# Kernel tuning notes

Hardware: AMD Instinct MI355X
Metric: run time of the kernel (lower is better)

## Reference

```python
import jax, jax.numpy as jnp
import numpy as np
from jax import lax

B, VLEN, H, DIM, C = 32, 2048, 1024, 1024, 32  # batch, value len, hidden_dim, dim, conv_out_channel


def setup_inputs() -> dict:
    key = jax.random.key(0)
    ks = jax.random.split(key, 13)
    s = 0.02
    return {
        "query": jax.random.normal(ks[0], (B, 1, H), dtype=jnp.float32),
        "value": jax.random.normal(ks[1], (B, VLEN, H), dtype=jnp.float32),
        "prev_attn": jax.random.uniform(ks[2], (B, VLEN), dtype=jnp.float32),
        "conv_w": jax.random.normal(ks[3], (C, 1, 3), dtype=jnp.float32) * s,   # Conv1d weight (out,in,k)
        "conv_b": jax.random.normal(ks[4], (C,), dtype=jnp.float32) * s,
        "w_loc": jax.random.normal(ks[5], (DIM, C), dtype=jnp.float32) * s,     # loc_projection (no bias)
        "w_q": jax.random.normal(ks[6], (DIM, H), dtype=jnp.float32) * s,       # query_projection (no bias)
        "w_v": jax.random.normal(ks[7], (DIM, H), dtype=jnp.float32) * s,       # value_projection (no bias)
        "bias": jax.random.uniform(ks[8], (DIM,), dtype=jnp.float32, minval=-0.1, maxval=0.1),
        "w_score": jax.random.normal(ks[9], (1, DIM), dtype=jnp.float32) * s,   # score_projection weight
        "b_score": jax.random.normal(ks[10], (1,), dtype=jnp.float32) * s,
        "w_out": jax.random.normal(ks[11], (H, 2 * H), dtype=jnp.float32) * s,  # out_projection weight
        "b_out": jax.random.normal(ks[12], (H,), dtype=jnp.float32) * s,
    }


def reference(query, value, prev_attn, conv_w, conv_b, w_loc, w_q, w_v, bias,
              w_score, b_score, w_out, b_out):
    # Location features: Conv1d(1 -> C, k=3, pad=1) over prev_attn, then transpose to (B, V, C)
    conv = lax.conv_general_dilated(
        prev_attn[:, None, :], conv_w, window_strides=(1,), padding=[(1, 1)],
        dimension_numbers=("NCH", "OIH", "NCH"),
    ) + conv_b[None, :, None]                       # (B, C, V)
    conv_feat = jnp.transpose(conv, (0, 2, 1))      # (B, V, C)

    qp = jnp.einsum("bqh,dh->bqd", query, w_q)      # (B, 1, DIM)
    vp = jnp.einsum("bvh,dh->bvd", value, w_v)      # (B, V, DIM)
    lp = jnp.einsum("bvc,dc->bvd", conv_feat, w_loc)

    e = jnp.tanh(qp + vp + lp + bias)               # (B, V, DIM), qp broadcasts over V
    score = jnp.einsum("bvd,d->bv", e, w_score[0]) + b_score[0]  # (B, V)

    # smoothing=True: sigmoid then normalize
    s = jax.nn.sigmoid(score)
    attn = s / jnp.sum(s, axis=-1, keepdims=True)   # (B, V)

    context = jnp.einsum("bv,bvh->bh", attn, value)               # (B, H)
    combined = jnp.concatenate([context[:, None, :], query], axis=2)  # (B, 1, 2H)
    output = jnp.einsum("bqk,hk->bqh", combined, w_out) + b_out       # (B, 1, H)
    return output, attn
```

## Files before the change

kernel.cpp:

```cpp
#include <hip/hip_runtime.h>
#include <hip/hip_bf16.h>
#include <math.h>

#define B_SZ 32
#define VLEN_SZ 2048
#define H_SZ 1024
#define DIM_SZ 1024
#define C_SZ 32

typedef float f32x4 __attribute__((ext_vector_type(4)));
typedef short s16x8 __attribute__((ext_vector_type(8)));
typedef short s16x4 __attribute__((ext_vector_type(4)));

__device__ __forceinline__ short f2bf(float f) {
  unsigned u = __float_as_uint(f);
  u = (u + 0x7fffu + ((u >> 16) & 1u)) >> 16;
  return (short)u;
}

__device__ __forceinline__ float bf2f(short s) {
  return __uint_as_float(((unsigned)(unsigned short)s) << 16);
}

__device__ __forceinline__ float fast_tanh(float x) {
  float z = __expf(2.0f * x);
  return 1.0f - 2.0f / (z + 1.0f);
}

__device__ __forceinline__ void ldg_lds16(const short* g, short* l) {
  __builtin_amdgcn_global_load_lds(
      (const __attribute__((address_space(1))) unsigned int*)g,
      (__attribute__((address_space(3))) unsigned int*)l, 16, 0, 0);
}

__global__ __launch_bounds__(256) void k_prep(
    const float* __restrict__ query, const float* __restrict__ w_q,
    const float* __restrict__ bias, const float* __restrict__ prev,
    const float* __restrict__ conv_w, const float* __restrict__ conv_b,
    const float* __restrict__ w_loc, const float* __restrict__ w_v,
    const float* __restrict__ value,
    float* __restrict__ qpb, short* __restrict__ cfb, short* __restrict__ wlocb,
    short* __restrict__ wvb, short* __restrict__ vb,
    float* __restrict__ score, float* __restrict__ context) {
  int bid = blockIdx.x;
  int t = threadIdx.x;
  if (bid < 8192) {
    int wid = bid * 4 + (t >> 6);
    int lane = t & 63;
    int d = wid >> 5;
    int b = wid & 31;
    const f32x4* q4 = (const f32x4*)(query + (size_t)b * H_SZ);
    const f32x4* w4 = (const f32x4*)(w_q + (size_t)d * H_SZ);
    float acc = 0.f;
#pragma unroll
    for (int it = 0; it < 4; ++it) {
      int k = it * 64 + lane;
      f32x4 a = q4[k], w = w4[k];
      acc += a[0] * w[0] + a[1] * w[1] + a[2] * w[2] + a[3] * w[3];
    }
#pragma unroll
    for (int off = 32; off; off >>= 1) acc += __shfl_xor(acc, off, 64);
    if (lane == 0) qpb[(size_t)b * DIM_SZ + d] = acc + bias[d];
  } else if (bid < 8448) {
    int r = (bid - 8192) * 256 + t;
    int v = r & (VLEN_SZ - 1);
    float p0 = prev[r];
    float pm = (v > 0) ? prev[r - 1] : 0.f;
    float pp = (v < VLEN_SZ - 1) ? prev[r + 1] : 0.f;
#pragma unroll
    for (int c = 0; c < C_SZ; ++c) {
      float f = conv_b[c] + pm * conv_w[c * 3 + 0] + p0 * conv_w[c * 3 + 1] + pp * conv_w[c * 3 + 2];
      cfb[(size_t)r * C_SZ + c] = f2bf(f);
    }
  } else if (bid < 8480) {
    int i = (bid - 8448) * 256 + t;
    f32x4 v = ((const f32x4*)w_loc)[i];
    s16x4 o;
    o[0] = f2bf(v[0]); o[1] = f2bf(v[1]); o[2] = f2bf(v[2]); o[3] = f2bf(v[3]);
    ((s16x4*)wlocb)[i] = o;
  } else if (bid < 9504) {
    int i = (bid - 8480) * 256 + t;
    f32x4 v = ((const f32x4*)w_v)[i];
    s16x4 o;
    o[0] = f2bf(v[0]); o[1] = f2bf(v[1]); o[2] = f2bf(v[2]); o[3] = f2bf(v[3]);
    ((s16x4*)wvb)[i] = o;
  } else if (bid < 9568) {
    int i = (bid - 9504) * 256 + t;
    ((f32x4*)score)[i] = (f32x4){0.f, 0.f, 0.f, 0.f};
  } else if (bid < 9600) {
    int i = (bid - 9568) * 256 + t;
    ((f32x4*)context)[i] = (f32x4){0.f, 0.f, 0.f, 0.f};
  } else {
    size_t i = (size_t)(bid - 9600) * 256 + t;
    f32x4 x0 = ((const f32x4*)value)[2 * i];
    f32x4 x1 = ((const f32x4*)value)[2 * i + 1];
    s16x8 o;
    o[0] = f2bf(x0[0]); o[1] = f2bf(x0[1]); o[2] = f2bf(x0[2]); o[3] = f2bf(x0[3]);
    o[4] = f2bf(x1[0]); o[5] = f2bf(x1[1]); o[6] = f2bf(x1[2]); o[7] = f2bf(x1[3]);
    ((s16x8*)vb)[i] = o;
  }
}

__global__ __launch_bounds__(256, 3) void k_score(
    const short* __restrict__ vb, const short* __restrict__ wvb,
    const short* __restrict__ wlocb, const short* __restrict__ cfb,
    const float* __restrict__ qpb, const float* __restrict__ w_score,
    float* __restrict__ score) {
  __shared__ short As[128 * 32];
  __shared__ short Bs[128 * 32];
  __shared__ float sred[4][64];

  int t = threadIdx.x;
  int w = t >> 6, l = t & 63;
  int q = l >> 4, l16 = l & 15;
  int bid = blockIdx.x;
  int x = bid & 7;
  int j = bid >> 3;
  int nt = j & 7;
  int mt = x * 64 + (j >> 3);
  int row0 = mt * 128;
  int d0 = nt * 128;
  int b = row0 >> 11;
  int wm = w >> 1, wn = w & 1;

  int lr = l >> 2;
  int kc = ((l & 3) ^ ((l >> 3) & 3)) * 8;

  const short* gA0 = vb + (size_t)(row0 + 32 * w + lr) * H_SZ + kc;
  const short* gA1 = vb + (size_t)(row0 + 32 * w + 16 + lr) * H_SZ + kc;
  const short* gB0 = wvb + (size_t)(d0 + 32 * w + lr) * H_SZ + kc;
  const short* gB1 = wvb + (size_t)(d0 + 32 * w + 16 + lr) * H_SZ + kc;
  short* lA0 = As + (32 * w) * 32;
  short* lA1 = As + (32 * w + 16) * 32;
  short* lB0 = Bs + (32 * w) * 32;
  short* lB1 = Bs + (32 * w + 16) * 32;

  int posA = (q ^ ((l16 >> 1) & 3)) * 8;

  f32x4 acc[4][4];
#pragma unroll
  for (int i = 0; i < 4; ++i)
#pragma unroll
    for (int jj = 0; jj < 4; ++jj) acc[i][jj] = (f32x4){0.f, 0.f, 0.f, 0.f};

  for (int kt = 0; kt <= 32; ++kt) {
    if (kt < 32) {
      int k0 = kt * 32;
      ldg_lds16(gA0 + k0, lA0);
      ldg_lds16(gA1 + k0, lA1);
      ldg_lds16(gB0 + k0, lB0);
      ldg_lds16(gB1 + k0, lB1);
    } else {
      ldg_lds16(cfb + (size_t)(row0 + 32 * w + lr) * C_SZ + kc, lA0);
      ldg_lds16(cfb + (size_t)(row0 + 32 * w + 16 + lr) * C_SZ + kc, lA1);
      ldg_lds16(wlocb + (size_t)(d0 + 32 * w + lr) * C_SZ + kc, lB0);
      ldg_lds16(wlocb + (size_t)(d0 + 32 * w + 16 + lr) * C_SZ + kc, lB1);
    }
    __syncthreads();

    s16x8 a[4], bb[4];
#pragma unroll
    for (int i = 0; i < 4; ++i)
      a[i] = *(const s16x8*)(As + (wm * 64 + i * 16 + l16) * 32 + posA);
#pragma unroll
    for (int jj = 0; jj < 4; ++jj)
      bb[jj] = *(const s16x8*)(Bs + (wn * 64 + jj * 16 + l16) * 32 + posA);
#pragma unroll
    for (int i = 0; i < 4; ++i)
#pragma unroll
      for (int jj = 0; jj < 4; ++jj)
        acc[i][jj] = __builtin_amdgcn_mfma_f32_16x16x32_bf16(a[i], bb[jj], acc[i][jj], 0, 0, 0);
    __syncthreads();
  }

  float qv[4], wv[4];
#pragma unroll
  for (int jj = 0; jj < 4; ++jj) {
    int d = d0 + wn * 64 + jj * 16 + l16;
    qv[jj] = qpb[(size_t)b * DIM_SZ + d];
    wv[jj] = w_score[d];
  }

#pragma unroll
  for (int i = 0; i < 4; ++i) {
#pragma unroll
    for (int r = 0; r < 4; ++r) {
      float part = 0.f;
#pragma unroll
      for (int jj = 0; jj < 4; ++jj)
        part += fast_tanh(acc[i][jj][r] + qv[jj]) * wv[jj];
      part += __shfl_xor(part, 1);
      part += __shfl_xor(part, 2);
      part += __shfl_xor(part, 4);
      part += __shfl_xor(part, 8);
      if (l16 == 0) sred[w][i * 16 + q * 4 + r] = part;
    }
  }
  __syncthreads();
  if (t < 128) {
    int half = t >> 6;
    float v = sred[half * 2][t & 63] + sred[half * 2 + 1][t & 63];
    atomicAdd(&score[row0 + t], v);
  }
}

__global__ __launch_bounds__(256) void k_ctx(
    const float* __restrict__ score, const float* __restrict__ b_score,
    const short* __restrict__ vb, float* __restrict__ attn_out,
    float* __restrict__ context) {
  __shared__ float als[VLEN_SZ];
  __shared__ float red[4];
  int b = blockIdx.x, vc = blockIdx.y, t = threadIdx.x;
  float bs = b_score[0];
  float sv[8];
  float lsum = 0.f;
  int v0 = t * 8;
#pragma unroll
  for (int k = 0; k < 8; ++k) {
    float ps = score[(size_t)b * VLEN_SZ + v0 + k] + bs;
    float s = 1.0f / (1.0f + __expf(-ps));
    sv[k] = s;
    lsum += s;
    als[v0 + k] = s;
  }
#pragma unroll
  for (int off = 32; off; off >>= 1) lsum += __shfl_xor(lsum, off, 64);
  if ((t & 63) == 0) red[t >> 6] = lsum;
  __syncthreads();
  float inv = 1.0f / (red[0] + red[1] + red[2] + red[3]);
  if (vc == 0) {
#pragma unroll
    for (int k = 0; k < 8; ++k)
      attn_out[(size_t)b * VLEN_SZ + v0 + k] = sv[k] * inv;
  }

  int p = t >> 7, tt = t & 127, h0 = tt * 8;
  int vbase = vc * 512 + p * 256;
  const short* vp = vb + ((size_t)b * VLEN_SZ + vbase) * H_SZ + h0;
  const float* av = als + vbase;
  float acc[8] = {0.f, 0.f, 0.f, 0.f, 0.f, 0.f, 0.f, 0.f};
#pragma unroll 4
  for (int v = 0; v < 256; ++v) {
    s16x8 xv = *(const s16x8*)(vp + (size_t)v * H_SZ);
    float a = av[v];
#pragma unroll
    for (int k = 0; k < 8; ++k) acc[k] += a * bf2f(xv[k]);
  }
#pragma unroll
  for (int k = 0; k < 8; ++k)
    atomicAdd(&context[(size_t)b * H_SZ + h0 + k], acc[k] * inv);
}

__global__ void k_out(const float* __restrict__ context, const float* __restrict__ query,
                      const float* __restrict__ w_out, const float* __restrict__ b_out,
                      float* __restrict__ out) {
  int wid = blockIdx.x * 4 + (threadIdx.x >> 6);
  int lane = threadIdx.x & 63;
  int h = wid >> 5;
  int b = wid & 31;
  const f32x4* w4 = (const f32x4*)(w_out + (size_t)h * 2048);
  const f32x4* c4 = (const f32x4*)(context + (size_t)b * H_SZ);
  const f32x4* q4 = (const f32x4*)(query + (size_t)b * H_SZ);
  float acc = 0.f;
#pragma unroll
  for (int it = 0; it < 8; ++it) {
    int k4 = it * 64 + lane;
    f32x4 w = w4[k4];
    f32x4 c = (k4 < 256) ? c4[k4] : q4[k4 - 256];
    acc += w[0] * c[0] + w[1] * c[1] + w[2] * c[2] + w[3] * c[3];
  }
#pragma unroll
  for (int off = 32; off; off >>= 1) acc += __shfl_xor(acc, off, 64);
  if (lane == 0) out[(size_t)b * H_SZ + h] = acc + b_out[h];
}

extern "C" void kernel_launch(void* const* d_in, const int* in_sizes, int n_in,
                              void* d_out, int out_size, void* d_ws, size_t ws_size,
                              hipStream_t stream) {
  const float* query   = (const float*)d_in[0];
  const float* value   = (const float*)d_in[1];
  const float* prev    = (const float*)d_in[2];
  const float* conv_w  = (const float*)d_in[3];
  const float* conv_b  = (const float*)d_in[4];
  const float* w_loc   = (const float*)d_in[5];
  const float* w_q     = (const float*)d_in[6];
  const float* w_v     = (const float*)d_in[7];
  const float* bias    = (const float*)d_in[8];
  const float* w_score = (const float*)d_in[9];
  const float* b_score = (const float*)d_in[10];
  const float* w_out   = (const float*)d_in[11];
  const float* b_out   = (const float*)d_in[12];

  float* out  = (float*)d_out;
  float* attn = out + B_SZ * H_SZ;

  char* ws = (char*)d_ws;
  float* score   = (float*)(ws);
  float* qpb     = (float*)(ws + (256 << 10));
  float* context = (float*)(ws + (384 << 10));
  short* wvb     = (short*)(ws + (512 << 10));
  short* wlocb   = (short*)(ws + (2560 << 10));
  short* cfb     = (short*)(ws + (3 << 20));
  short* vb      = (short*)(ws + (8 << 20));

  k_prep<<<42368, 256, 0, stream>>>(query, w_q, bias, prev, conv_w, conv_b,
                                    w_loc, w_v, value,
                                    qpb, cfb, wlocb, wvb, vb, score, context);
  k_score<<<4096, 256, 0, stream>>>(vb, wvb, wlocb, cfb, qpb, w_score, score);
  k_ctx<<<dim3(B_SZ, 4), 256, 0, stream>>>(score, b_score, vb, attn, context);
  k_out<<<(B_SZ * H_SZ) / 4, 256, 0, stream>>>(context, query, w_out, b_out, out);
}
```

Before: 637.7 us.

## Drop bf16 value pre-conversion; load fp32 value directly into score GEMM

Removes the separate pass that converted the whole value tensor to bf16 in the prep kernel. The score GEMM now streams fp32 value tiles into LDS and packs them to bf16 by truncation when forming the MFMA operands. The context kernel reads fp32 value directly with a doubled grid. The aim is to avoid writing and re-reading a large bf16 copy, at the cost of double the LDS footprint and A-tile global traffic in the GEMM, plus truncation instead of round-to-nearest.

```diff
diff --git a/kernel.cpp b/kernel.cpp
--- a/kernel.cpp
+++ b/kernel.cpp
@@ -11,6 +11,7 @@
 typedef float f32x4 __attribute__((ext_vector_type(4)));
 typedef short s16x8 __attribute__((ext_vector_type(8)));
 typedef short s16x4 __attribute__((ext_vector_type(4)));
+typedef unsigned int u32x4 __attribute__((ext_vector_type(4)));
 
 __device__ __forceinline__ short f2bf(float f) {
   unsigned u = __float_as_uint(f);
@@ -22,12 +23,16 @@
   return __uint_as_float(((unsigned)(unsigned short)s) << 16);
 }
 
+__device__ __forceinline__ unsigned pack2(float a, float b) {
+  return __builtin_amdgcn_perm(__float_as_uint(b), __float_as_uint(a), 0x07060302u);
+}
+
 __device__ __forceinline__ float fast_tanh(float x) {
   float z = __expf(2.0f * x);
   return 1.0f - 2.0f / (z + 1.0f);
 }
 
-__device__ __forceinline__ void ldg_lds16(const short* g, short* l) {
+__device__ __forceinline__ void ldg_lds16(const void* g, void* l) {
   __builtin_amdgcn_global_load_lds(
       (const __attribute__((address_space(1))) unsigned int*)g,
       (__attribute__((address_space(3))) unsigned int*)l, 16, 0, 0);
@@ -38,10 +43,8 @@
     const float* __restrict__ bias, const float* __restrict__ prev,
     const float* __restrict__ conv_w, const float* __restrict__ conv_b,
     const float* __restrict__ w_loc, const float* __restrict__ w_v,
-    const float* __restrict__ value,
-    float* __restrict__ qpb, short* __restrict__ cfb, short* __restrict__ wlocb,
-    short* __restrict__ wvb, short* __restrict__ vb,
-    float* __restrict__ score, float* __restrict__ context) {
+    float* __restrict__ qpb, float* __restrict__ cff, short* __restrict__ wlocb,
+    short* __restrict__ wvb, float* __restrict__ score, float* __restrict__ context) {
   int bid = blockIdx.x;
   int t = threadIdx.x;
   if (bid < 8192) {
@@ -67,11 +70,14 @@
     float p0 = prev[r];
     float pm = (v > 0) ? prev[r - 1] : 0.f;
     float pp = (v < VLEN_SZ - 1) ? prev[r + 1] : 0.f;
-#pragma unroll
-    for (int c = 0; c < C_SZ; ++c) {
-      float f = conv_b[c] + pm * conv_w[c * 3 + 0] + p0 * conv_w[c * 3 + 1] + pp * conv_w[c * 3 + 2];
-      cfb[(size_t)r * C_SZ + c] = f2bf(f);
-    }
+    float o[C_SZ];
+#pragma unroll
+    for (int c = 0; c < C_SZ; ++c)
+      o[c] = conv_b[c] + pm * conv_w[c * 3 + 0] + p0 * conv_w[c * 3 + 1] + pp * conv_w[c * 3 + 2];
+    f32x4* dst = (f32x4*)(cff + (size_t)r * C_SZ);
+#pragma unroll
+    for (int g = 0; g < 8; ++g)
+      dst[g] = (f32x4){o[4 * g], o[4 * g + 1], o[4 * g + 2], o[4 * g + 3]};
   } else if (bid < 8480) {
     int i = (bid - 8448) * 256 + t;
     f32x4 v = ((const f32x4*)w_loc)[i];
@@ -87,26 +93,18 @@
   } else if (bid < 9568) {
     int i = (bid - 9504) * 256 + t;
     ((f32x4*)score)[i] = (f32x4){0.f, 0.f, 0.f, 0.f};
-  } else if (bid < 9600) {
+  } else {
     int i = (bid - 9568) * 256 + t;
     ((f32x4*)context)[i] = (f32x4){0.f, 0.f, 0.f, 0.f};
-  } else {
-    size_t i = (size_t)(bid - 9600) * 256 + t;
-    f32x4 x0 = ((const f32x4*)value)[2 * i];
-    f32x4 x1 = ((const f32x4*)value)[2 * i + 1];
-    s16x8 o;
-    o[0] = f2bf(x0[0]); o[1] = f2bf(x0[1]); o[2] = f2bf(x0[2]); o[3] = f2bf(x0[3]);
-    o[4] = f2bf(x1[0]); o[5] = f2bf(x1[1]); o[6] = f2bf(x1[2]); o[7] = f2bf(x1[3]);
-    ((s16x8*)vb)[i] = o;
-  }
-}
-
-__global__ __launch_bounds__(256, 3) void k_score(
-    const short* __restrict__ vb, const short* __restrict__ wvb,
-    const short* __restrict__ wlocb, const short* __restrict__ cfb,
+  }
+}
+
+__global__ __launch_bounds__(256, 4) void k_score(
+    const float* __restrict__ value, const short* __restrict__ wvb,
+    const short* __restrict__ wlocb, const float* __restrict__ cff,
     const float* __restrict__ qpb, const float* __restrict__ w_score,
     float* __restrict__ score) {
-  __shared__ short As[128 * 32];
+  __shared__ float As[128 * 32];
   __shared__ short Bs[128 * 32];
   __shared__ float sred[4][64];
 
@@ -123,19 +121,26 @@
   int b = row0 >> 11;
   int wm = w >> 1, wn = w & 1;
 
+  int ar = l >> 3;
+  int ac = (l & 7) ^ ar;
+  const float* gA[4];
+  float* lA[4];
+#pragma unroll
+  for (int s = 0; s < 4; ++s) {
+    gA[s] = value + (size_t)(row0 + 32 * w + 8 * s + ar) * H_SZ + ac * 4;
+    lA[s] = As + (32 * w + 8 * s) * 32;
+  }
   int lr = l >> 2;
   int kc = ((l & 3) ^ ((l >> 3) & 3)) * 8;
-
-  const short* gA0 = vb + (size_t)(row0 + 32 * w + lr) * H_SZ + kc;
-  const short* gA1 = vb + (size_t)(row0 + 32 * w + 16 + lr) * H_SZ + kc;
   const short* gB0 = wvb + (size_t)(d0 + 32 * w + lr) * H_SZ + kc;
   const short* gB1 = wvb + (size_t)(d0 + 32 * w + 16 + lr) * H_SZ + kc;
-  short* lA0 = As + (32 * w) * 32;
-  short* lA1 = As + (32 * w + 16) * 32;
   short* lB0 = Bs + (32 * w) * 32;
   short* lB1 = Bs + (32 * w + 16) * 32;
 
-  int posA = (q ^ ((l16 >> 1) & 3)) * 8;
+  int h7 = l16 & 7;
+  int pA0 = ((2 * q) ^ h7) * 4;
+  int pA1 = ((2 * q + 1) ^ h7) * 4;
+  int posB = (q ^ ((l16 >> 1) & 3)) * 8;
 
   f32x4 acc[4][4];
 #pragma unroll
@@ -146,13 +151,14 @@
   for (int kt = 0; kt <= 32; ++kt) {
     if (kt < 32) {
       int k0 = kt * 32;
-      ldg_lds16(gA0 + k0, lA0);
-      ldg_lds16(gA1 + k0, lA1);
-      ldg_lds16(gB0 + k0, lB0);
-      ldg_lds16(gB1 + k0, lB1);
+#pragma unroll
+      for (int s = 0; s < 4; ++s) ldg_lds16(gA[s] + k0, lA[s]);
+      ldg_lds16(gB0 + (size_t)k0, lB0);
+      ldg_lds16(gB1 + (size_t)k0, lB1);
     } else {
-      ldg_lds16(cfb + (size_t)(row0 + 32 * w + lr) * C_SZ + kc, lA0);
-      ldg_lds16(cfb + (size_t)(row0 + 32 * w + 16 + lr) * C_SZ + kc, lA1);
+#pragma unroll
+      for (int s = 0; s < 4; ++s)
+        ldg_lds16(cff + (size_t)(row0 + 32 * w + 8 * s + ar) * C_SZ + ac * 4, lA[s]);
       ldg_lds16(wlocb + (size_t)(d0 + 32 * w + lr) * C_SZ + kc, lB0);
       ldg_lds16(wlocb + (size_t)(d0 + 32 * w + 16 + lr) * C_SZ + kc, lB1);
     }
@@ -160,11 +166,20 @@
 
     s16x8 a[4], bb[4];
 #pragma unroll
-    for (int i = 0; i < 4; ++i)
-      a[i] = *(const s16x8*)(As + (wm * 64 + i * 16 + l16) * 32 + posA);
+    for (int i = 0; i < 4; ++i) {
+      const float* rowp = As + (wm * 64 + i * 16 + l16) * 32;
+      f32x4 f0 = *(const f32x4*)(rowp + pA0);
+      f32x4 f1 = *(const f32x4*)(rowp + pA1);
+      u32x4 pk;
+      pk[0] = pack2(f0[0], f0[1]);
+      pk[1] = pack2(f0[2], f0[3]);
+      pk[2] = pack2(f1[0], f1[1]);
+      pk[3] = pack2(f1[2], f1[3]);
+      a[i] = *(s16x8*)&pk;
+    }
 #pragma unroll
     for (int jj = 0; jj < 4; ++jj)
-      bb[jj] = *(const s16x8*)(Bs + (wn * 64 + jj * 16 + l16) * 32 + posA);
+      bb[jj] = *(const s16x8*)(Bs + (wn * 64 + jj * 16 + l16) * 32 + posB);
 #pragma unroll
     for (int i = 0; i < 4; ++i)
 #pragma unroll
@@ -206,7 +221,7 @@
 
 __global__ __launch_bounds__(256) void k_ctx(
     const float* __restrict__ score, const float* __restrict__ b_score,
-    const short* __restrict__ vb, float* __restrict__ attn_out,
+    const float* __restrict__ value, float* __restrict__ attn_out,
     float* __restrict__ context) {
   __shared__ float als[VLEN_SZ];
   __shared__ float red[4];
@@ -234,20 +249,20 @@
       attn_out[(size_t)b * VLEN_SZ + v0 + k] = sv[k] * inv;
   }
 
-  int p = t >> 7, tt = t & 127, h0 = tt * 8;
-  int vbase = vc * 512 + p * 256;
-  const short* vp = vb + ((size_t)b * VLEN_SZ + vbase) * H_SZ + h0;
+  int h0 = t * 4;
+  int vbase = vc * 256;
+  const float* vp = value + ((size_t)b * VLEN_SZ + vbase) * H_SZ + h0;
   const float* av = als + vbase;
-  float acc[8] = {0.f, 0.f, 0.f, 0.f, 0.f, 0.f, 0.f, 0.f};
-#pragma unroll 4
+  f32x4 acc = (f32x4){0.f, 0.f, 0.f, 0.f};
+#pragma unroll 8
   for (int v = 0; v < 256; ++v) {
-    s16x8 xv = *(const s16x8*)(vp + (size_t)v * H_SZ);
+    f32x4 xv = *(const f32x4*)(vp + (size_t)v * H_SZ);
     float a = av[v];
-#pragma unroll
-    for (int k = 0; k < 8; ++k) acc[k] += a * bf2f(xv[k]);
-  }
-#pragma unroll
-  for (int k = 0; k < 8; ++k)
+    acc[0] += a * xv[0]; acc[1] += a * xv[1];
+    acc[2] += a * xv[2]; acc[3] += a * xv[3];
+  }
+#pragma unroll
+  for (int k = 0; k < 4; ++k)
     atomicAdd(&context[(size_t)b * H_SZ + h0 + k], acc[k] * inv);
 }
 
@@ -300,13 +315,11 @@
   float* context = (float*)(ws + (384 << 10));
   short* wvb     = (short*)(ws + (512 << 10));
   short* wlocb   = (short*)(ws + (2560 << 10));
-  short* cfb     = (short*)(ws + (3 << 20));
-  short* vb      = (short*)(ws + (8 << 20));
-
-  k_prep<<<42368, 256, 0, stream>>>(query, w_q, bias, prev, conv_w, conv_b,
-                                    w_loc, w_v, value,
-                                    qpb, cfb, wlocb, wvb, vb, score, context);
-  k_score<<<4096, 256, 0, stream>>>(vb, wvb, wlocb, cfb, qpb, w_score, score);
-  k_ctx<<<dim3(B_SZ, 4), 256, 0, stream>>>(score, b_score, vb, attn, context);
+  float* cff     = (float*)(ws + (3 << 20));
+
+  k_prep<<<9600, 256, 0, stream>>>(query, w_q, bias, prev, conv_w, conv_b,
+                                   w_loc, w_v, qpb, cff, wlocb, wvb, score, context);
+  k_score<<<4096, 256, 0, stream>>>(value, wvb, wlocb, cff, qpb, w_score, score);
+  k_ctx<<<dim3(B_SZ, 8), 256, 0, stream>>>(score, b_score, value, attn, context);
   k_out<<<(B_SZ * H_SZ) / 4, 256, 0, stream>>>(context, query, w_out, b_out, out);
 }
```

Result: no change. 632.4 us (-0.8%).
